# Performance work log

Measured on AMD Instinct MI355X. Metric: run time of the kernel, lower is better.

The kernel has to match this reference:

```python
import jax, jax.numpy as jnp
import numpy as np

B, L, D = 4, 2048, 1024
MD = D // 4      # memory_dim = dim // 4
K = 5            # kernel_size
DIL = 1          # dilation
EPS = 1e-6


def rmsnorm(x, w):
    return w * x * jax.lax.rsqrt(jnp.mean(x * x, axis=-1, keepdims=True) + EPS)


def setup_inputs() -> dict:
    key = jax.random.key(0)
    ks = jax.random.split(key, 16)
    n = lambda k, shape, s=0.02: jax.random.normal(k, shape, jnp.float32) * s
    return dict(
        x=jax.random.normal(ks[0], (B, L, D), jnp.float32),
        memory_state=jnp.zeros((B, MD), jnp.float32),
        norm_w=jnp.ones((D,), jnp.float32),
        dw_kernel=n(ks[1], (D, 1, K), 0.1),   # depthwise conv [O,I/g,K]
        dw_bias=jnp.zeros((D,), jnp.float32),
        pw_kernel=n(ks[2], (D, D)),           # 1x1 conv as [out,in]
        pw_bias=jnp.zeros((D,), jnp.float32),
        Win_w=n(ks[3], (MD, D)), Win_b=jnp.zeros((MD,), jnp.float32),
        Wf_w=n(ks[4], (MD, D + MD)), Wf_b=jnp.ones((MD,), jnp.float32),  # forget bias init 1.0
        Wu_w=n(ks[5], (MD, D + MD)), Wu_b=jnp.zeros((MD,), jnp.float32),
        Wo_w=n(ks[6], (D, D + MD)), Wo_b=jnp.zeros((D,), jnp.float32),
        router_w=n(ks[7], (2, D)), router_b=jnp.zeros((2,), jnp.float32),
        e0_w1=n(ks[8], (D, D)), e0_b1=jnp.zeros((D,), jnp.float32),
        e0_w2=n(ks[9], (D, D)), e0_b2=jnp.zeros((D,), jnp.float32),
        e1_w1=n(ks[10], (D, D)), e1_b1=jnp.zeros((D,), jnp.float32),
        e1_w2=n(ks[11], (D, D)), e1_b2=jnp.zeros((D,), jnp.float32),
        fnorm_w=jnp.ones((D,), jnp.float32),
        down_w=n(ks[12], (D // 4, D)), down_b=jnp.zeros((D // 4,), jnp.float32),
        up_w=n(ks[13], (D, D // 4)), up_b=jnp.zeros((D,), jnp.float32),
    )


def reference(x, memory_state, norm_w, dw_kernel, dw_bias, pw_kernel, pw_bias,
              Win_w, Win_b, Wf_w, Wf_b, Wu_w, Wu_b, Wo_w, Wo_b,
              router_w, router_b, e0_w1, e0_b1, e0_w2, e0_b2,
              e1_w1, e1_b1, e1_w2, e1_b2, fnorm_w, down_w, down_b, up_w, up_b):
    resid = x
    xn = rmsnorm(x, norm_w)                              # [B,L,D]

    # --- causal depthwise conv (left pad (K-1)*DIL == torch pad-both + slice[:L]) + pointwise ---
    P = (K - 1) * DIL
    xc = jnp.swapaxes(xn, 1, 2)                          # [B,D,L]
    xc = jax.lax.conv_general_dilated(
        xc, dw_kernel, window_strides=(1,), padding=[(P, 0)],
        rhs_dilation=(DIL,), dimension_numbers=('NCH', 'OIH', 'NCH'),
        feature_group_count=D) + dw_bias[None, :, None]
    x_conv = jnp.einsum('bdl,ed->ble', xc, pw_kernel) + pw_bias  # [B,L,D]

    # --- structured state recurrence (gated, scan over time) ---
    Wf_x, Wf_m = Wf_w[:, :D], Wf_w[:, D:]
    Wu_x, Wu_m = Wu_w[:, :D], Wu_w[:, D:]
    Wo_x, Wo_m = Wo_w[:, :D], Wo_w[:, D:]
    # precompute all x-dependent projections: [L,B,*]
    fx = jnp.einsum('bld,md->lbm', xn, Wf_x) + Wf_b
    ux = jnp.einsum('bld,md->lbm', xn, Wu_x) + Wu_b
    ox = jnp.einsum('bld,ed->lbe', xn, Wo_x) + Wo_b
    xm = jax.nn.silu(jnp.einsum('bld,md->lbm', xn, Win_w) + Win_b)
    xt = jnp.swapaxes(xn, 0, 1)                          # [L,B,D]

    def step(m, inp):
        fx_t, ux_t, ox_t, xm_t, x_t = inp
        f = jax.nn.sigmoid(fx_t + m @ Wf_m.T)
        u = jax.nn.sigmoid(ux_t + m @ Wu_m.T)
        m2 = f * m + u * xm_t
        out = x_t + ox_t + m2 @ Wo_m.T
        return m2, out

    new_mem, rec = jax.lax.scan(step, memory_state, (fx, ux, ox, xm, xt))
    x_rec = jnp.swapaxes(rec, 0, 1)                      # [B,L,D]

    y = x_conv + x_rec

    # --- enhanced gated fusion (2-expert soft MoE) ---
    r = jax.nn.softmax(y @ router_w.T + router_b, axis=-1)   # [B,L,2]
    e0 = jax.nn.silu(y @ e0_w1.T + e0_b1) @ e0_w2.T + e0_b2
    e1 = jax.nn.silu(y @ e1_w1.T + e1_b1) @ e1_w2.T + e1_b2
    y = rmsnorm(y + r[..., 0:1] * e0 + r[..., 1:2] * e1, fnorm_w)

    # --- low-rank FF (exact GELU) + residual ---
    ff = jax.nn.gelu(y @ down_w.T + down_b, approximate=False) @ up_w.T + up_b
    out = y + ff + resid
    return out, new_mem
```

## Files before the change

### kernel.cpp

```cpp
#include <hip/hip_runtime.h>
#include <hip/hip_bf16.h>

#define DD 1024
#define MDD 256
#define LL 2048
#define BB 4
#define NROWS (BB*LL)
#define NCH 8
#define TCH (LL/NCH)

typedef short bf16x8 __attribute__((ext_vector_type(8)));
typedef float f32x4 __attribute__((ext_vector_type(4)));
typedef int   i32x4 __attribute__((ext_vector_type(4)));

__device__ __forceinline__ short f2b(float x){
  __hip_bfloat16 h = __float2bfloat16(x);
  return *reinterpret_cast<short*>(&h);
}
__device__ __forceinline__ float b2f(short s){
  return __uint_as_float(((unsigned)(unsigned short)s) << 16);
}
__device__ __forceinline__ float frcp(float x){
#if __has_builtin(__builtin_amdgcn_rcpf)
  return __builtin_amdgcn_rcpf(x);
#else
  float r; asm("v_rcp_f32 %0, %1" : "=v"(r) : "v"(x)); return r;
#endif
}
__device__ __forceinline__ float fsigmoid(float x){
  return frcp(1.f + __expf(-x));
}
__device__ __forceinline__ float sel4(f32x4 a, int kg){
  float lo = (kg & 1) ? a[1] : a[0];
  float hi = (kg & 1) ? a[3] : a[2];
  return (kg & 2) ? hi : lo;
}

struct CvtDesc {
  const float* src; const float* src2; short* dstb; float* dstf;
  int n, cols, sld, soff, dld, mode;
};
struct CvtArgs { CvtDesc d[20]; };

__global__ __launch_bounds__(256) void cvt_all(CvtArgs a){
  int di = blockIdx.x >> 6;
  CvtDesc d = a.d[di];
  int base = (blockIdx.x & 63)*256 + threadIdx.x;
  for (int i = base; i < d.n; i += 64*256){
    int r = i / d.cols, c = i - r*d.cols;
    float v = d.src[(size_t)r*d.sld + d.soff + c];
    if (d.mode == 2) v += d.src2[i];
    if (d.mode == 0) d.dstb[(size_t)r*d.dld + c] = f2b(v);
    else             d.dstf[i] = v;
  }
}

__global__ __launch_bounds__(256) void rmsnorm_k(const float* __restrict__ x,
                                                 const float* __restrict__ w,
                                                 short* __restrict__ xn){
  int row = blockIdx.x, tid = threadIdx.x;
  const float* xr = x + (size_t)row*DD;
  float4 v = *(const float4*)&xr[tid*4];
  float ss = v.x*v.x + v.y*v.y + v.z*v.z + v.w*v.w;
  __shared__ float red[256];
  red[tid] = ss; __syncthreads();
  for (int s = 128; s > 0; s >>= 1){ if (tid < s) red[tid] += red[tid+s]; __syncthreads(); }
  float scale = rsqrtf(red[0]/(float)DD + 1e-6f);
  const float* wr = w + tid*4;
  short4 o;
  o.x = f2b(v.x*wr[0]*scale); o.y = f2b(v.y*wr[1]*scale);
  o.z = f2b(v.z*wr[2]*scale); o.w = f2b(v.w*wr[3]*scale);
  *(short4*)&xn[(size_t)row*2048 + tid*4] = o;
}

__global__ __launch_bounds__(256) void dwconv_k(const short* __restrict__ xnA,
                                                const float* __restrict__ dwk,
                                                const float* __restrict__ dwb,
                                                short* __restrict__ xcA){
  size_t i = (size_t)blockIdx.x*256 + threadIdx.x;
  int d = (int)(i & (DD-1));
  int l = (int)((i >> 10) & (LL-1));
  int b = (int)(i >> 21);
  float acc = dwb[d];
  const float* kk = dwk + d*5;
  #pragma unroll
  for (int k = 0; k < 5; ++k){
    int ll = l + k - 4;
    if (ll >= 0) acc += b2f(xnA[((size_t)(b*LL + ll))*2048 + d]) * kk[k];
  }
  xcA[((size_t)(b*LL + l))*2048 + 1024 + d] = f2b(acc);
}

struct Job {
  const short* A; const short* Bw; const float* bias;
  const float* add0; const float* add1; void* Cf; short* C2;
  int N, K, lda, ldb, bn, nblocks, bm0, cstart, act, outmode, permute, remap, type;
};
struct PipeArgs { Job j[8]; int njobs; };

__global__ __launch_bounds__(512, 2) void pipe_k(
    const float* __restrict__ fxu, const short* __restrict__ Wfu,
    const float* __restrict__ m0, float* __restrict__ mstate,
    short* __restrict__ m2all, float* __restrict__ newmem,
    int t0, int nsteps, int has_scan, PipeArgs pa){
  __shared__ __align__(16) short lds[8192];
  const int tid = threadIdx.x, lane = tid & 63, w = tid >> 6;
  const int r0 = lane & 15, kg = lane >> 4;

  if (!has_scan || blockIdx.x != 0){
    int jb = (int)blockIdx.x - has_scan;
    int ji = 0;
    while (jb >= pa.j[ji].nblocks){ jb -= pa.j[ji].nblocks; ++ji; }
    const Job J = pa.j[ji];

    if (J.type == 1){
      float* red  = (float*)lds;
      float* red2 = red + 512;
      float* y = (float*)J.Cf;
      const short* e0 = J.A; const short* e1 = J.Bw;
      const float* rw = J.bias; const float* rb = J.add0; const float* fw = J.add1;
      short* y2bf = J.C2;
      int c = J.bm0;
      float2 w0  = *(const float2*)&rw[tid*2];
      float2 w1  = *(const float2*)&rw[1024 + tid*2];
      float2 fw2 = *(const float2*)&fw[tid*2];
      float rb0 = rb[0], rb1 = rb[1];
      for (int rr = 0; rr < 4; ++rr){
        int rl = jb*4 + rr;
        int b = rl >> 8, t = c*256 + (rl & 255);
        size_t base = ((size_t)b*LL + t)*1024 + tid*2;
        float2 vy = *(const float2*)&y[base];
        short2 s0 = *(const short2*)&e0[base];
        short2 s1 = *(const short2*)&e1[base];
        float d0 = vy.x*w0.x + vy.y*w0.y;
        float d1 = vy.x*w1.x + vy.y*w1.y;
        red[tid] = d0; red2[tid] = d1; __syncthreads();
        for (int s = 256; s > 0; s >>= 1){
          if (tid < s){ red[tid] += red[tid+s]; red2[tid] += red2[tid+s]; }
          __syncthreads();
        }
        float l0 = red[0] + rb0, l1 = red2[0] + rb1;
        float p0 = 1.f/(1.f + __expf(l1 - l0));
        float p1 = 1.f - p0;
        float c0 = vy.x + p0*b2f(s0.x) + p1*b2f(s1.x);
        float c1 = vy.y + p0*b2f(s0.y) + p1*b2f(s1.y);
        float ss = c0*c0 + c1*c1;
        __syncthreads();
        red[tid] = ss; __syncthreads();
        for (int s = 256; s > 0; s >>= 1){
          if (tid < s) red[tid] += red[tid+s];
          __syncthreads();
        }
        float scale = rsqrtf(red[0]/1024.f + 1e-6f);
        float o0 = c0*fw2.x*scale, o1 = c1*fw2.y*scale;
        float2 ov; ov.x = o0; ov.y = o1;
        *(float2*)&y[base] = ov;
        short2 ob; ob.x = f2b(o0); ob.y = f2b(o1);
        *(short2*)&y2bf[base] = ob;
        __syncthreads();
      }
      return;
    }

    int bnidx = jb % J.bn;
    int lb2 = jb / J.bn;
    int bm;
    if (J.remap == 0) bm = J.bm0 + lb2;
    else { int c = J.cstart + (lb2 >> 3); int q = lb2 & 7; bm = (q>>1)*16 + c*2 + (q&1); }
    short* As = lds;
    short* Bs = lds + 4096;
    int wm = (w >> 2)*64, wn = (w & 3)*32;
    f32x4 acc[4][2];
    #pragma unroll
    for (int i = 0; i < 4; ++i)
      #pragma unroll
      for (int j = 0; j < 2; ++j)
        #pragma unroll
        for (int r = 0; r < 4; ++r) acc[i][j][r] = 0.f;

    const short* ag = J.A  + (size_t)(bm*128    + (tid >> 2))*J.lda + (tid & 3)*8;
    const short* bg = J.Bw + (size_t)(bnidx*128 + (tid >> 2))*J.ldb + (tid & 3)*8;

    for (int k0 = 0; k0 < J.K; k0 += 32){
      __builtin_amdgcn_global_load_lds((const __attribute__((address_space(1))) void*)(ag + k0),
                                       (__attribute__((address_space(3))) void*)&As[w*512], 16, 0, 0);
      __builtin_amdgcn_global_load_lds((const __attribute__((address_space(1))) void*)(bg + k0),
                                       (__attribute__((address_space(3))) void*)&Bs[w*512], 16, 0, 0);
      __syncthreads();
      bf16x8 av[4], bv[2];
      #pragma unroll
      for (int i = 0; i < 4; ++i) av[i] = *(const bf16x8*)&As[(wm + i*16 + r0)*32 + kg*8];
      #pragma unroll
      for (int j = 0; j < 2; ++j) bv[j] = *(const bf16x8*)&Bs[(wn + j*16 + r0)*32 + kg*8];
      #pragma unroll
      for (int i = 0; i < 4; ++i)
        #pragma unroll
        for (int j = 0; j < 2; ++j)
          acc[i][j] = __builtin_amdgcn_mfma_f32_16x16x32_bf16(av[i], bv[j], acc[i][j], 0, 0, 0);
      __syncthreads();
    }
    #pragma unroll
    for (int i = 0; i < 4; ++i){
      #pragma unroll
      for (int j = 0; j < 2; ++j){
        int gc = bnidx*128 + wn + j*16 + r0;
        float bvv = J.bias ? J.bias[gc] : 0.f;
        #pragma unroll
        for (int r = 0; r < 4; ++r){
          int gr = bm*128 + wm + i*16 + kg*4 + r;
          float v = acc[i][j][r] + bvv;
          if (J.act == 1) v = v / (1.f + __expf(-v));
          else if (J.act == 2) v = 0.5f*v*(1.f + erff(v*0.70710678118f));
          size_t orow = J.permute ? (size_t)((gr & 3)*LL + (gr >> 2)) : (size_t)gr;
          size_t oi = orow*(size_t)J.N + gc;
          if (J.add0) v += J.add0[oi];
          if (J.add1) v += J.add1[oi];
          if (J.outmode == 0) ((float*)J.Cf)[oi] = v;
          else if (J.outmode == 2) ((short*)J.Cf)[oi] = f2b(v);
          else {
            float nv = ((float*)J.Cf)[oi] + v;
            ((float*)J.Cf)[oi] = nv;
            J.C2[oi] = f2b(nv);
          }
        }
      }
    }
    return;
  }

  short* mA0 = lds;
  short* mA1 = lds + 1088;
  const int j0 = w*32 + r0;

  bf16x8 bw[2][2][8];
  #pragma unroll
  for (int fu = 0; fu < 2; ++fu)
    #pragma unroll
    for (int p = 0; p < 2; ++p)
      #pragma unroll
      for (int kt = 0; kt < 8; ++kt){
        i32x4 ld = *(const i32x4*)&Wfu[(size_t)(fu*256 + w*32 + p*16 + r0)*256 + kt*32 + kg*8];
        asm volatile("" : "+v"(ld));
        bw[fu][p][kt] = __builtin_bit_cast(bf16x8, ld);
      }

  const float* msrc = (t0 == 0) ? m0 : mstate;
  float m_reg0 = msrc[kg*256 + j0];
  float m_reg1 = msrc[kg*256 + j0 + 16];

  const float* pfu;
  const float* px;
  short* pm = m2all + (size_t)t0*1024 + kg*256 + j0;
  float cf0, cf1, cu0, cu1, xmc0, xmc1, nx0, nx1;
  {
    const float* b0p = fxu + ((size_t)kg*LL + t0)*768 + j0;
    cf0 = b0p[0];    cf1 = b0p[16];
    cu0 = b0p[256];  cu1 = b0p[272];
    float tx0 = b0p[512], tx1 = b0p[528];
    xmc0 = tx0*fsigmoid(tx0);  xmc1 = tx1*fsigmoid(tx1);
    nx0 = b0p[768 + 512];  nx1 = b0p[768 + 528];
    pfu = b0p + 768;
    px  = b0p + 2*768 + 512;
  }
  mA0[kg*272 + j0]      = f2b(m_reg0);
  mA0[kg*272 + j0 + 16] = f2b(m_reg1);
  __syncthreads();

  const short* mac = mA0;
  short*       man = mA1;

#define SCAN_STEP(DO_FU, DO_X)                                                         \
  {                                                                                    \
    bf16x8 af[8];                                                                      \
    _Pragma("unroll")                                                                  \
    for (int kt = 0; kt < 8; ++kt)                                                     \
      af[kt] = *(const bf16x8*)&mac[(r0 & 3)*272 + kt*32 + kg*8];                      \
    float xmn0 = nx0*fsigmoid(nx0);                                                    \
    float xmn1 = nx1*fsigmoid(nx1);                                                    \
    __builtin_amdgcn_s_setprio(1);                                                     \
    f32x4 aF0 = {0.f,0.f,0.f,0.f}, aF1 = {0.f,0.f,0.f,0.f};                            \
    f32x4 aU0 = {0.f,0.f,0.f,0.f}, aU1 = {0.f,0.f,0.f,0.f};                            \
    _Pragma("unroll")                                                                  \
    for (int kt = 0; kt < 8; ++kt){                                                    \
      aF0 = __builtin_amdgcn_mfma_f32_16x16x32_bf16(af[kt], bw[0][0][kt], aF0, 0, 0, 0); \
      aF1 = __builtin_amdgcn_mfma_f32_16x16x32_bf16(af[kt], bw[0][1][kt], aF1, 0, 0, 0); \
      aU0 = __builtin_amdgcn_mfma_f32_16x16x32_bf16(af[kt], bw[1][0][kt], aU0, 0, 0, 0); \
      aU1 = __builtin_amdgcn_mfma_f32_16x16x32_bf16(af[kt], bw[1][1][kt], aU1, 0, 0, 0); \
    }                                                                                  \
    __builtin_amdgcn_s_setprio(0);                                                     \
    float gF0 = sel4(aF0, kg), gF1 = sel4(aF1, kg);                                    \
    float gU0 = sel4(aU0, kg), gU1 = sel4(aU1, kg);                                    \
    float f0 = fsigmoid(gF0 + cf0);                                                    \
    float f1 = fsigmoid(gF1 + cf1);                                                    \
    float u0 = fsigmoid(gU0 + cu0);                                                    \
    float u1 = fsigmoid(gU1 + cu1);                                                    \
    m_reg0 = f0*m_reg0 + u0*xmc0;                                                      \
    m_reg1 = f1*m_reg1 + u1*xmc1;                                                      \
    short mb0 = f2b(m_reg0), mb1 = f2b(m_reg1);                                        \
    pm[0] = mb0; pm[16] = mb1; pm += 1024;                                             \
    xmc0 = xmn0; xmc1 = xmn1;                                                          \
    if (DO_FU){                                                                        \
      cf0 = pfu[0];    cf1 = pfu[16];                                                  \
      cu0 = pfu[256];  cu1 = pfu[272];                                                 \
      pfu += 768;                                                                      \
    }                                                                                  \
    if (DO_X){                                                                         \
      nx0 = px[0]; nx1 = px[16]; px += 768;                                            \
    }                                                                                  \
    man[kg*272 + j0]      = mb0;                                                       \
    man[kg*272 + j0 + 16] = mb1;                                                       \
    asm volatile("s_waitcnt lgkmcnt(0)" ::: "memory");                                 \
    __builtin_amdgcn_sched_barrier(0);                                                 \
    __builtin_amdgcn_s_barrier();                                                      \
    __builtin_amdgcn_sched_barrier(0);                                                 \
    { const short* tmp_ = mac; mac = man; man = (short*)tmp_; }                        \
  }

  for (int t = 0; t < nsteps - 2; ++t) SCAN_STEP(1, 1)
  SCAN_STEP(1, 0)
  SCAN_STEP(0, 0)
#undef SCAN_STEP

  mstate[kg*256 + j0]      = m_reg0;
  mstate[kg*256 + j0 + 16] = m_reg1;
  if (t0 + nsteps == LL){
    newmem[kg*256 + j0]      = m_reg0;
    newmem[kg*256 + j0 + 16] = m_reg1;
  }
}

extern "C" void kernel_launch(void* const* d_in, const int* in_sizes, int n_in,
                              void* d_out, int out_size, void* d_ws, size_t ws_size,
                              hipStream_t stream){
  (void)in_sizes; (void)n_in; (void)out_size; (void)ws_size;
  const float* x     = (const float*)d_in[0];
  const float* mem0  = (const float*)d_in[1];
  const float* normw = (const float*)d_in[2];
  const float* dwk   = (const float*)d_in[3];
  const float* dwb   = (const float*)d_in[4];
  const float* pw    = (const float*)d_in[5];
  const float* pwb   = (const float*)d_in[6];
  const float* Win_w = (const float*)d_in[7];
  const float* Win_b = (const float*)d_in[8];
  const float* Wf_w  = (const float*)d_in[9];
  const float* Wf_b  = (const float*)d_in[10];
  const float* Wu_w  = (const float*)d_in[11];
  const float* Wu_b  = (const float*)d_in[12];
  const float* Wo_w  = (const float*)d_in[13];
  const float* Wo_b  = (const float*)d_in[14];
  const float* rw    = (const float*)d_in[15];
  const float* rb    = (const float*)d_in[16];
  const float* e0w1  = (const float*)d_in[17];
  const float* e0b1  = (const float*)d_in[18];
  const float* e0w2  = (const float*)d_in[19];
  const float* e0b2  = (const float*)d_in[20];
  const float* e1w1  = (const float*)d_in[21];
  const float* e1b1  = (const float*)d_in[22];
  const float* e1w2  = (const float*)d_in[23];
  const float* e1b2  = (const float*)d_in[24];
  const float* fnw   = (const float*)d_in[25];
  const float* dnw   = (const float*)d_in[26];
  const float* dnb   = (const float*)d_in[27];
  const float* upw   = (const float*)d_in[28];
  const float* upb   = (const float*)d_in[29];

  char* ws = (char*)d_ws;
  size_t off = 0;
  auto alloc = [&](size_t bytes)->char*{
    char* p = ws + off; off += (bytes + 255) & ~(size_t)255; return p;
  };
  short* A2       = (short*)alloc((size_t)NROWS*2048*2);
  short* B2       = (short*)alloc((size_t)1024*2048*2);
  short* W_fxuwin = (short*)alloc((size_t)768*1024*2);
  short* W_fum    = (short*)alloc((size_t)512*256*2);
  short* W_om     = (short*)alloc((size_t)1024*256*2);
  short* W_e01    = (short*)alloc((size_t)2048*1024*2);
  short* W_e0w2   = (short*)alloc((size_t)1024*1024*2);
  short* W_e1w2   = (short*)alloc((size_t)1024*1024*2);
  short* W_down   = (short*)alloc((size_t)256*1024*2);
  short* W_up     = (short*)alloc((size_t)1024*256*2);
  float* bias768  = (float*)alloc(768*4);
  float* bias2    = (float*)alloc(1024*4);
  float* bias01   = (float*)alloc(2048*4);
  float* mstate   = (float*)alloc(1024*4);
  float* fxu      = (float*)alloc((size_t)NROWS*768*4);
  float* ybuf     = (float*)alloc((size_t)NROWS*DD*4);
  short* m2all    = (short*)alloc((size_t)NROWS*MDD*2);
  short* ybf      = (short*)alloc((size_t)NROWS*DD*2);
  short* e0v      = (short*)alloc((size_t)NROWS*DD*2);
  short* e1v      = (short*)alloc((size_t)NROWS*DD*2);
  short* h01      = (short*)alloc((size_t)NROWS*2048*2);
  short* hd       = (short*)alloc((size_t)NROWS*MDD*2);
  float* newmem   = (float*)d_out + (size_t)NROWS*DD;

  CvtArgs ca;
  auto D0 = [&](const float* s, short* db, int rows, int cols, int sld, int soff, int dld){
    return CvtDesc{s, nullptr, db, nullptr, rows*cols, cols, sld, soff, dld, 0};
  };
  auto D1 = [&](const float* s, float* df, int n){
    return CvtDesc{s, nullptr, nullptr, df, n, n, 0, 0, 0, 1};
  };
  ca.d[0]  = D0(Wo_w,  B2,                1024, 1024, 1280, 0,    2048);
  ca.d[1]  = D0(pw,    B2+1024,           1024, 1024, 1024, 0,    2048);
  ca.d[2]  = D0(Wf_w,  W_fxuwin,           256, 1024, 1280, 0,    1024);
  ca.d[3]  = D0(Wu_w,  W_fxuwin+256*1024,  256, 1024, 1280, 0,    1024);
  ca.d[4]  = D0(Win_w, W_fxuwin+512*1024,  256, 1024, 1024, 0,    1024);
  ca.d[5]  = D0(Wf_w,  W_fum,              256,  256, 1280, 1024, 256);
  ca.d[6]  = D0(Wu_w,  W_fum+256*256,      256,  256, 1280, 1024, 256);
  ca.d[7]  = D0(Wo_w,  W_om,              1024,  256, 1280, 1024, 256);
  ca.d[8]  = D0(e0w1,  W_e01,             1024, 1024, 1024, 0,    1024);
  ca.d[9]  = D0(e1w1,  W_e01+1024*1024,   1024, 1024, 1024, 0,    1024);
  ca.d[10] = D0(e0w2,  W_e0w2,            1024, 1024, 1024, 0,    1024);
  ca.d[11] = D0(e1w2,  W_e1w2,            1024, 1024, 1024, 0,    1024);
  ca.d[12] = D0(dnw,   W_down,             256, 1024, 1024, 0,    1024);
  ca.d[13] = D0(upw,   W_up,              1024,  256,  256, 0,    256);
  ca.d[14] = D1(Wf_b,  bias768,       256);
  ca.d[15] = D1(Wu_b,  bias768+256,   256);
  ca.d[16] = D1(Win_b, bias768+512,   256);
  ca.d[17] = CvtDesc{Wo_b, pwb, nullptr, bias2, 1024, 1024, 0, 0, 0, 2};
  ca.d[18] = D1(e0b1,  bias01,       1024);
  ca.d[19] = D1(e1b1,  bias01+1024,  1024);
  cvt_all<<<20*64, 256, 0, stream>>>(ca);

  rmsnorm_k<<<NROWS, 256, 0, stream>>>(x, normw, A2);
  dwconv_k<<<(NROWS*DD)/256, 256, 0, stream>>>(A2, dwk, dwb, A2);

  auto JG = [&](const short* A, const short* Bw, const float* bias,
                const float* a0, const float* a1, void* Cf, short* C2,
                int N, int K, int lda, int ldb, int bn, int nbm, int bm0, int cstart,
                int act, int outm, int perm, int remap)->Job{
    return Job{A, Bw, bias, a0, a1, Cf, C2, N, K, lda, ldb, bn, nbm*bn, bm0, cstart,
               act, outm, perm, remap, 0};
  };
  auto G2j   = [&](int cstart, int nch)->Job{
    return JG(A2, W_fxuwin, bias768, nullptr, nullptr, fxu, nullptr,
              768, 1024, 2048, 1024, 6, nch*8, 0, cstart, 0, 0, 0, 1); };
  Job G34j   = JG(A2, B2, bias2, x, nullptr, ybuf, nullptr,
                  1024, 2048, 2048, 2048, 8, 64, 0, 0, 0, 0, 0, 0);
  auto G5j   = [&](int k)->Job{
    return JG(m2all, W_om, nullptr, nullptr, nullptr, ybuf, ybf,
              1024, 256, 256, 256, 8, 8, k*8, 0, 0, 3, 1, 0); };
  auto E1j   = [&](int k)->Job{
    return JG(ybf, W_e01, bias01, nullptr, nullptr, h01, nullptr,
              2048, 1024, 1024, 1024, 16, 8, 0, k, 1, 2, 0, 1); };
  auto E2aj  = [&](int k)->Job{
    return JG(h01, W_e0w2, e0b2, nullptr, nullptr, e0v, nullptr,
              1024, 1024, 2048, 1024, 8, 8, 0, k, 0, 2, 0, 1); };
  auto E2bj  = [&](int k)->Job{
    return JG(h01+1024, W_e1w2, e1b2, nullptr, nullptr, e1v, nullptr,
              1024, 1024, 2048, 1024, 8, 8, 0, k, 0, 2, 0, 1); };
  auto CBj   = [&](int k)->Job{
    return Job{(const short*)e0v, (const short*)e1v, rw, rb, fnw, ybuf, ybf,
               0, 0, 0, 0, 0, 256, k, 0, 0, 0, 0, 0, 1}; };
  auto G10j  = [&](int k)->Job{
    return JG(ybf, W_down, dnb, nullptr, nullptr, hd, nullptr,
              256, 1024, 1024, 1024, 2, 8, 0, k, 2, 2, 0, 1); };
  auto G11j  = [&](int k)->Job{
    return JG(hd, W_up, upb, ybuf, x, (float*)d_out, nullptr,
              1024, 256, 256, 256, 8, 8, 0, k, 0, 0, 0, 1); };

  auto launch = [&](int t0, int nsteps, std::initializer_list<Job> jobs){
    PipeArgs pa{}; int nb = 0, nj = 0;
    for (const Job& j : jobs){ pa.j[nj++] = j; nb += j.nblocks; }
    pa.njobs = nj;
    int has = nsteps > 0 ? 1 : 0;
    pipe_k<<<has + nb, 512, 0, stream>>>(fxu, W_fum, mem0, mstate, m2all, newmem,
                                         t0, nsteps, has, pa);
  };

  launch(0, 0, { G2j(0, 1) });
  launch(0*TCH, TCH, { G2j(1, 7), G34j });
  launch(1*TCH, TCH, { G5j(0) });
  launch(2*TCH, TCH, { G5j(1), E1j(0) });
  launch(3*TCH, TCH, { G5j(2), E1j(1), E2aj(0), E2bj(0) });
  launch(4*TCH, TCH, { G5j(3), E1j(2), E2aj(1), E2bj(1), CBj(0) });
  launch(5*TCH, TCH, { G5j(4), E1j(3), E2aj(2), E2bj(2), CBj(1), G10j(0) });
  launch(6*TCH, TCH, { G5j(5), E1j(4), E2aj(3), E2bj(3), CBj(2), G10j(1), G11j(0) });
  launch(7*TCH, TCH, { G5j(6), E1j(5), E2aj(4), E2bj(4), CBj(3), G10j(2), G11j(1) });
  launch(0, 0, { G5j(7), E1j(6), E2aj(5), E2bj(5), CBj(4), G10j(3), G11j(2) });
  launch(0, 0, { E1j(7), E2aj(6), E2bj(6), CBj(5), G10j(4), G11j(3) });
  launch(0, 0, { E2aj(7), E2bj(7), CBj(6), G10j(5), G11j(4) });
  launch(0, 0, { CBj(7), G10j(6), G11j(5) });
  launch(0, 0, { G10j(7), G11j(6) });
  launch(0, 0, { G11j(7) });
}
```

Measured before the change: 2.003 ms.

## Spread input-projection GEMMs across scan chunks and pad registers in scan launches

The fxu projection (G2) and the conv-pointwise GEMM (G34) are now split per time chunk and issued one chunk ahead across the pipelined launches, instead of being front-loaded into the first scan launch. This spreads the GEMM work so it overlaps the sequential scan through every chunk. A templated padding variant holds 40 dummy VGPRs live in launches that run the scan, which raises register use so fewer blocks share a CU with the latency-critical scan block. The padding also lowers occupancy for the co-scheduled GEMM blocks, and the remap logic for G34 now depends on chunk indexing being correct.

```diff
diff --git a/kernel.cpp b/kernel.cpp
--- a/kernel.cpp
+++ b/kernel.cpp
@@ -1,5 +1,6 @@
 #include <hip/hip_runtime.h>
 #include <hip/hip_bf16.h>
+#include <initializer_list>
 
 #define DD 1024
 #define MDD 256
@@ -96,8 +97,9 @@
   const float* add0; const float* add1; void* Cf; short* C2;
   int N, K, lda, ldb, bn, nblocks, bm0, cstart, act, outmode, permute, remap, type;
 };
-struct PipeArgs { Job j[8]; int njobs; };
-
+struct PipeArgs { Job j[12]; int njobs; };
+
+template<int PAD>
 __global__ __launch_bounds__(512, 2) void pipe_k(
     const float* __restrict__ fxu, const short* __restrict__ Wfu,
     const float* __restrict__ m0, float* __restrict__ mstate,
@@ -106,6 +108,21 @@
   __shared__ __align__(16) short lds[8192];
   const int tid = threadIdx.x, lane = tid & 63, w = tid >> 6;
   const int r0 = lane & 15, kg = lane >> 4;
+
+  i32x4 p0, p1, p2, p3, p4, p5, p6, p7, p8, p9;
+  if (PAD){
+    p0 = i32x4{0,0,0,0}; asm volatile("" : "+v"(p0));
+    p1 = i32x4{0,0,0,0}; asm volatile("" : "+v"(p1));
+    p2 = i32x4{0,0,0,0}; asm volatile("" : "+v"(p2));
+    p3 = i32x4{0,0,0,0}; asm volatile("" : "+v"(p3));
+    p4 = i32x4{0,0,0,0}; asm volatile("" : "+v"(p4));
+    p5 = i32x4{0,0,0,0}; asm volatile("" : "+v"(p5));
+    p6 = i32x4{0,0,0,0}; asm volatile("" : "+v"(p6));
+    p7 = i32x4{0,0,0,0}; asm volatile("" : "+v"(p7));
+    p8 = i32x4{0,0,0,0}; asm volatile("" : "+v"(p8));
+    p9 = i32x4{0,0,0,0}; asm volatile("" : "+v"(p9));
+  }
+#define PAD_SINK() if (PAD) asm volatile("" :: "v"(p0),"v"(p1),"v"(p2),"v"(p3),"v"(p4),"v"(p5),"v"(p6),"v"(p7),"v"(p8),"v"(p9))
 
   if (!has_scan || blockIdx.x != 0){
     int jb = (int)blockIdx.x - has_scan;
@@ -140,10 +157,10 @@
           __syncthreads();
         }
         float l0 = red[0] + rb0, l1 = red2[0] + rb1;
-        float p0 = 1.f/(1.f + __expf(l1 - l0));
-        float p1 = 1.f - p0;
-        float c0 = vy.x + p0*b2f(s0.x) + p1*b2f(s1.x);
-        float c1 = vy.y + p0*b2f(s0.y) + p1*b2f(s1.y);
+        float pp0 = 1.f/(1.f + __expf(l1 - l0));
+        float pp1 = 1.f - pp0;
+        float c0 = vy.x + pp0*b2f(s0.x) + pp1*b2f(s1.x);
+        float c1 = vy.y + pp0*b2f(s0.y) + pp1*b2f(s1.y);
         float ss = c0*c0 + c1*c1;
         __syncthreads();
         red[tid] = ss; __syncthreads();
@@ -159,6 +176,7 @@
         *(short2*)&y2bf[base] = ob;
         __syncthreads();
       }
+      PAD_SINK();
       return;
     }
 
@@ -225,6 +243,7 @@
         }
       }
     }
+    PAD_SINK();
     return;
   }
 
@@ -327,6 +346,8 @@
     newmem[kg*256 + j0]      = m_reg0;
     newmem[kg*256 + j0 + 16] = m_reg1;
   }
+  PAD_SINK();
+#undef PAD_SINK
 }
 
 extern "C" void kernel_launch(void* const* d_in, const int* in_sizes, int n_in,
@@ -432,11 +453,12 @@
     return Job{A, Bw, bias, a0, a1, Cf, C2, N, K, lda, ldb, bn, nbm*bn, bm0, cstart,
                act, outm, perm, remap, 0};
   };
-  auto G2j   = [&](int cstart, int nch)->Job{
+  auto G2j   = [&](int cstart)->Job{
     return JG(A2, W_fxuwin, bias768, nullptr, nullptr, fxu, nullptr,
-              768, 1024, 2048, 1024, 6, nch*8, 0, cstart, 0, 0, 0, 1); };
-  Job G34j   = JG(A2, B2, bias2, x, nullptr, ybuf, nullptr,
-                  1024, 2048, 2048, 2048, 8, 64, 0, 0, 0, 0, 0, 0);
+              768, 1024, 2048, 1024, 6, 8, 0, cstart, 0, 0, 0, 1); };
+  auto G34j  = [&](int k)->Job{
+    return JG(A2, B2, bias2, x, nullptr, ybuf, nullptr,
+              1024, 2048, 2048, 2048, 8, 8, 0, k, 0, 0, 0, 1); };
   auto G5j   = [&](int k)->Job{
     return JG(m2all, W_om, nullptr, nullptr, nullptr, ybuf, ybf,
               1024, 256, 256, 256, 8, 8, k*8, 0, 0, 3, 1, 0); };
@@ -464,19 +486,23 @@
     for (const Job& j : jobs){ pa.j[nj++] = j; nb += j.nblocks; }
     pa.njobs = nj;
     int has = nsteps > 0 ? 1 : 0;
-    pipe_k<<<has + nb, 512, 0, stream>>>(fxu, W_fum, mem0, mstate, m2all, newmem,
-                                         t0, nsteps, has, pa);
+    if (has)
+      pipe_k<1><<<has + nb, 512, 0, stream>>>(fxu, W_fum, mem0, mstate, m2all, newmem,
+                                              t0, nsteps, has, pa);
+    else
+      pipe_k<0><<<nb, 512, 0, stream>>>(fxu, W_fum, mem0, mstate, m2all, newmem,
+                                        t0, nsteps, 0, pa);
   };
 
-  launch(0, 0, { G2j(0, 1) });
-  launch(0*TCH, TCH, { G2j(1, 7), G34j });
-  launch(1*TCH, TCH, { G5j(0) });
-  launch(2*TCH, TCH, { G5j(1), E1j(0) });
-  launch(3*TCH, TCH, { G5j(2), E1j(1), E2aj(0), E2bj(0) });
-  launch(4*TCH, TCH, { G5j(3), E1j(2), E2aj(1), E2bj(1), CBj(0) });
-  launch(5*TCH, TCH, { G5j(4), E1j(3), E2aj(2), E2bj(2), CBj(1), G10j(0) });
-  launch(6*TCH, TCH, { G5j(5), E1j(4), E2aj(3), E2bj(3), CBj(2), G10j(1), G11j(0) });
-  launch(7*TCH, TCH, { G5j(6), E1j(5), E2aj(4), E2bj(4), CBj(3), G10j(2), G11j(1) });
+  launch(0, 0, { G2j(0) });
+  launch(0*TCH, TCH, { G2j(1), G34j(0) });
+  launch(1*TCH, TCH, { G2j(2), G34j(1), G5j(0) });
+  launch(2*TCH, TCH, { G2j(3), G34j(2), G5j(1), E1j(0) });
+  launch(3*TCH, TCH, { G2j(4), G34j(3), G5j(2), E1j(1), E2aj(0), E2bj(0) });
+  launch(4*TCH, TCH, { G2j(5), G34j(4), G5j(3), E1j(2), E2aj(1), E2bj(1), CBj(0) });
+  launch(5*TCH, TCH, { G2j(6), G34j(5), G5j(4), E1j(3), E2aj(2), E2bj(2), CBj(1), G10j(0) });
+  launch(6*TCH, TCH, { G2j(7), G34j(6), G5j(5), E1j(4), E2aj(3), E2bj(3), CBj(2), G10j(1), G11j(0) });
+  launch(7*TCH, TCH, { G34j(7), G5j(6), E1j(5), E2aj(4), E2bj(4), CBj(3), G10j(2), G11j(1) });
   launch(0, 0, { G5j(7), E1j(6), E2aj(5), E2bj(5), CBj(4), G10j(3), G11j(2) });
   launch(0, 0, { E1j(7), E2aj(6), E2bj(6), CBj(5), G10j(4), G11j(3) });
   launch(0, 0, { E2aj(7), E2bj(7), CBj(6), G10j(5), G11j(4) });
```

Measured after the change: 1.982 ms. No clear change (-1.0%).
